# Kernel tuning notes

Hardware: AMD Instinct MI355X
Metric: run time of the kernel (lower is better)

Reference implementation:

```python
import jax, jax.numpy as jnp
import numpy as np

B, G, D, H, DH, L, M, FF = 8, 20000, 256, 8, 32, 4, 128, 1024
MASK_ID = -10.0


def _ortho(rng, m, d):
    # Gaussian orthogonal random features (performer_pytorch, scaling=0)
    rows = []
    n = 0
    while n < m:
        q, _ = np.linalg.qr(rng.standard_normal((d, d)))
        rows.append(q.T)
        n += d
    W = np.concatenate(rows)[:m]
    mult = np.linalg.norm(rng.standard_normal((m, d)), axis=1)
    return (mult[:, None] * W).astype(np.float32)


def setup_inputs() -> dict:
    rng = np.random.default_rng(0)
    p = lambda *s: (0.02 * rng.standard_normal(s)).astype(np.float32)
    z = lambda *s: np.zeros(s, np.float32)
    o = lambda *s: np.ones(s, np.float32)
    inp = dict(
        x=rng.standard_normal((B, G)).astype(np.float32),
        gene_emb=p(G, D),
        se_w1=p(G, 256), se_b1=z(256), se_w2=p(256, D), se_b2=z(D),
        proj_w1=p(D, FF), proj_b1=z(FF), proj_w2=p(FF, D), proj_b2=z(D),
        ln1_g=o(L, D), ln1_b=z(L, D),
        wq=p(L, D, D), wk=p(L, D, D), wv=p(L, D, D), wo=p(L, D, D), bo=z(L, D),
        ln2_g=o(L, D), ln2_b=z(L, D),
        ff_w1=p(L, D, FF), ff_b1=z(L, FF), ff_w2=p(L, FF, D), ff_b2=z(L, D),
        feat_proj=np.stack([_ortho(rng, M, DH) for _ in range(L)]),
        norm_g=o(D), norm_b=z(D),
        head_w1=p(D, FF), head_b1=z(FF), head_w2=p(FF, 1), head_b2=z(1),
    )
    return {k: jnp.asarray(v) for k, v in inp.items()}


def _ln(x, g, b, eps=1e-5):
    mu = jnp.mean(x, -1, keepdims=True)
    var = jnp.mean((x - mu) ** 2, -1, keepdims=True)
    return (x - mu) * jax.lax.rsqrt(var + eps) * g + b


def _softmax_kernel(x, proj, is_query, eps=1e-4):
    # FAVOR+ positive softmax kernel features (performer_pytorch softmax_kernel)
    d = x.shape[-1]
    ratio = proj.shape[0] ** -0.5
    dn = d ** -0.25
    dd = jnp.einsum('bhnd,md->bhnm', x * dn, proj)
    diag = 0.5 * jnp.sum(x * x, -1, keepdims=True) * (dn * dn)
    if is_query:
        m = jnp.max(dd, axis=-1, keepdims=True)
    else:
        m = jnp.max(dd, axis=(-1, -2), keepdims=True)
    return ratio * (jnp.exp(dd - diag - m) + eps)


def _forward(x, gene_emb, se_w1, se_b1, se_w2, se_b2, proj_w1, proj_b1,
             proj_w2, proj_b2, ln1_g, ln1_b, wq, wk, wv, wo, bo, ln2_g, ln2_b,
             ff_w1, ff_b1, ff_w2, ff_b2, feat_proj, norm_g, norm_b,
             head_w1, head_b1, head_w2, head_b2):
    # Rotary Expression Embedding
    inv_freq = 1.0 / (100.0 ** (jnp.arange(0, D, 2, dtype=jnp.float32) / D))
    freqs = x[:, :, None] * inv_freq                        # [B,G,D/2]
    ree = jnp.concatenate([jnp.sin(freqs), jnp.cos(freqs)], -1)
    ree = jnp.where((x == MASK_ID)[:, :, None], 0.0, ree)
    # sample embedding + gene token embedding
    samp = jax.nn.relu(x @ se_w1 + se_b1) @ se_w2 + se_b2   # [B,D]
    h = gene_emb[None] + ree + samp[:, None, :]             # [B,G,D]
    h = jax.nn.relu(h @ proj_w1 + proj_b1) @ proj_w2 + proj_b2
    for l in range(L):
        x0 = h
        a = _ln(x0, ln1_g[l], ln1_b[l])
        q = (a @ wq[l]).reshape(B, G, H, DH).transpose(0, 2, 1, 3)
        k = (a @ wk[l]).reshape(B, G, H, DH).transpose(0, 2, 1, 3)
        v = (a @ wv[l]).reshape(B, G, H, DH).transpose(0, 2, 1, 3)
        qp = _softmax_kernel(q, feat_proj[l], True)         # [B,H,G,M]
        kp = _softmax_kernel(k, feat_proj[l], False)
        ksum = kp.sum(2)                                    # [B,H,M]
        dinv = 1.0 / jnp.einsum('bhnm,bhm->bhn', qp, ksum)
        ctx = jnp.einsum('bhnm,bhnd->bhmd', kp, v)          # [B,H,M,DH]
        o_ = jnp.einsum('bhnm,bhmd,bhn->bhnd', qp, ctx, dinv)
        o_ = o_.transpose(0, 2, 1, 3).reshape(B, G, D)
        y = x0 + (o_ @ wo[l] + bo[l])                       # attn residual
        f = _ln(y, ln2_g[l], ln2_b[l])
        y = y + (jax.nn.gelu(f @ ff_w1[l] + ff_b1[l], approximate=False) @ ff_w2[l] + ff_b2[l])
        h = y + h                                           # outer residual
    h = _ln(h, norm_g, norm_b)
    pred = (jax.nn.relu(h @ head_w1 + head_b1) @ head_w2 + head_b2)[..., 0]
    return jax.nn.relu(pred)                                # [B,G]


def reference(x, gene_emb, se_w1, se_b1, se_w2, se_b2, proj_w1, proj_b1,
              proj_w2, proj_b2, ln1_g, ln1_b, wq, wk, wv, wo, bo, ln2_g,
              ln2_b, ff_w1, ff_b1, ff_w2, ff_b2, feat_proj, norm_g, norm_b,
              head_w1, head_b1, head_w2, head_b2):
    return _forward(x, gene_emb, se_w1, se_b1, se_w2, se_b2, proj_w1, proj_b1,
                    proj_w2, proj_b2, ln1_g, ln1_b, wq, wk, wv, wo, bo, ln2_g,
                    ln2_b, ff_w1, ff_b1, ff_w2, ff_b2, feat_proj, norm_g,
                    norm_b, head_w1, head_b1, head_w2, head_b2)
```

## Files before the change

### kernel.cpp

```cpp
#include <hip/hip_runtime.h>

#define Bb 8
#define Gg 20000
#define Dd 256
#define Hh 8
#define DHh 32
#define Ll 4
#define Mm 128
#define FFf 1024
#define QKVS 768
#define NBLK 192
#define NSLOT 105

typedef __attribute__((ext_vector_type(8))) short bf16x8;
typedef __attribute__((ext_vector_type(4))) float f32x4;

#define DN    0.4204482076268573f
#define DN2H  0.088388347648318447f
#define RATIO 0.08838834764831845f
#define EPSK  1e-4f

__device__ __forceinline__ float geluf(float x) {
    return 0.5f * x * (1.0f + erff(x * 0.70710678118654752f));
}
__device__ __forceinline__ float bf2f(ushort u) {
    union { uint i; float f; } v; v.i = ((uint)u) << 16; return v.f;
}
__device__ __forceinline__ ushort f2bf(float f) {
    union { float f; uint i; } v; v.f = f;
    uint i = v.i;
    return (ushort)((i + 0x7FFFu + ((i >> 16) & 1u)) >> 16);
}
__device__ __forceinline__ void gload16(const void* g, void* l) {
    __builtin_amdgcn_global_load_lds(
        (const __attribute__((address_space(1))) void*)g,
        (__attribute__((address_space(3))) void*)l, 16, 0, 0);
}

__global__ __launch_bounds__(256) void k_wt4(const float* __restrict__ wk,
    const float* __restrict__ wv, const float* __restrict__ wq,
    const float* __restrict__ wo, ushort* __restrict__ Wt)
{
    const int z = blockIdx.z, l = z >> 2, wh = z & 3;
    const float* src = (wh == 0) ? wk : (wh == 1) ? wv : (wh == 2) ? wq : wo;
    src += (size_t)l * 65536;
    ushort* d = Wt + (size_t)l * 786432 + (size_t)wh * 65536;
    __shared__ float tl[32][33];
    const int n0 = blockIdx.x * 32, k0 = blockIdx.y * 32;
    const int tx = threadIdx.x & 31, ty = threadIdx.x >> 5;
#pragma unroll
    for (int i = 0; i < 4; i++)
        tl[ty + i*8][tx] = src[(size_t)(k0 + ty + i*8) * 256 + n0 + tx];
    __syncthreads();
#pragma unroll
    for (int i = 0; i < 4; i++)
        d[(size_t)(n0 + ty + i*8) * 256 + k0 + tx] = f2bf(tl[tx][ty + i*8]);
}

__global__ __launch_bounds__(256) void k_wtA(const float* __restrict__ ff1,
    const float* __restrict__ pw1, const float* __restrict__ hw1,
    ushort* __restrict__ Wt)
{
    const int z = blockIdx.z;
    const float* src; ushort* d;
    if (z < 4)      { src = ff1 + (size_t)z*262144; d = Wt + (size_t)z*786432 + 262144; }
    else if (z == 4){ src = pw1; d = Wt + (size_t)4*786432; }
    else            { src = hw1; d = Wt + (size_t)4*786432 + 524288; }
    __shared__ float tl[32][33];
    const int n0 = blockIdx.x * 32, k0 = blockIdx.y * 32;
    const int tx = threadIdx.x & 31, ty = threadIdx.x >> 5;
#pragma unroll
    for (int i = 0; i < 4; i++)
        tl[ty + i*8][tx] = src[(size_t)(k0 + ty + i*8) * 1024 + n0 + tx];
    __syncthreads();
#pragma unroll
    for (int i = 0; i < 4; i++)
        d[(size_t)(n0 + ty + i*8) * 256 + k0 + tx] = f2bf(tl[tx][ty + i*8]);
}

__global__ __launch_bounds__(256) void k_wtB(const float* __restrict__ ff2,
    const float* __restrict__ pw2, ushort* __restrict__ Wt)
{
    const int z = blockIdx.z;
    const float* src; ushort* d;
    if (z < 4) { src = ff2 + (size_t)z*262144; d = Wt + (size_t)z*786432 + 524288; }
    else       { src = pw2; d = Wt + (size_t)4*786432 + 262144; }
    __shared__ float tl[32][33];
    const int n0 = blockIdx.x * 32, k0 = blockIdx.y * 32;
    const int tx = threadIdx.x & 31, ty = threadIdx.x >> 5;
#pragma unroll
    for (int i = 0; i < 4; i++)
        tl[ty + i*8][tx] = src[(size_t)(k0 + ty + i*8) * 256 + n0 + tx];
    __syncthreads();
#pragma unroll
    for (int i = 0; i < 4; i++)
        d[(size_t)(n0 + ty + i*8) * 1024 + k0 + tx] = f2bf(tl[tx][ty + i*8]);
}

__global__ __launch_bounds__(256) void k_pcast(const float* __restrict__ src,
    ushort* __restrict__ dst, int n)
{
    int i = blockIdx.x*256 + threadIdx.x;
    if (i < n) dst[i] = f2bf(src[i]);
}

__global__ __launch_bounds__(128) void k_pn(const float* __restrict__ featp,
    float* __restrict__ pnorm)
{
    const int l = blockIdx.x, t = threadIdx.x;
    const float* p = featp + (size_t)l*4096 + t*32;
    float s = 0.f;
#pragma unroll
    for (int d = 0; d < 32; d++) s += p[d]*p[d];
#pragma unroll
    for (int off = 1; off < 64; off <<= 1) s = fmaxf(s, __shfl_xor(s, off));
    __shared__ float sm2[2];
    if ((t & 63) == 0) sm2[t >> 6] = s;
    __syncthreads();
    if (t == 0) pnorm[l] = sqrtf(fmaxf(sm2[0], sm2[1]));
}

__global__ __launch_bounds__(512) void gemm_bf(
    const ushort* __restrict__ A, const ushort* __restrict__ Bt,
    const float* __restrict__ bias, ushort* __restrict__ C,
    int Mrows, int N, int K, int act)
{
    __shared__ ushort As[8192];
    __shared__ ushort Bs[8192];
    const int t = threadIdx.x;
    const int l = t & 63, wid = t >> 6;
    const int lr = l & 15, q = l >> 4;
    const int wm = wid >> 2, wn = wid & 3;
    const int row0 = blockIdx.y * 128, col0 = blockIdx.x * 128;

    const int sar = min(row0 + wid*16 + lr, Mrows - 1);
    const ushort* gA = A  + (size_t)sar * K + q*8;
    const ushort* gB = Bt + (size_t)(col0 + wid*16 + lr) * K + q*8;
    ushort* lA = As + wid*1024;
    ushort* lB = Bs + wid*1024;

    f32x4 acc[4][2] = {};

    for (int k0 = 0; k0 < K; k0 += 64) {
        __syncthreads();
        gload16(gA + k0,      lA);
        gload16(gA + k0 + 32, lA + 512);
        gload16(gB + k0,      lB);
        gload16(gB + k0 + 32, lB + 512);
        __syncthreads();
#pragma unroll
        for (int kg = 0; kg < 2; kg++) {
            bf16x8 af[4];
#pragma unroll
            for (int mi = 0; mi < 4; mi++)
                af[mi] = *(const bf16x8*)&As[((wm*4 + mi)*2 + kg)*512 + l*8];
#pragma unroll
            for (int ni = 0; ni < 2; ni++) {
                bf16x8 bv = *(const bf16x8*)&Bs[((wn*2 + ni)*2 + kg)*512 + l*8];
#pragma unroll
                for (int mi = 0; mi < 4; mi++)
                    acc[mi][ni] = __builtin_amdgcn_mfma_f32_16x16x32_bf16(
                        af[mi], bv, acc[mi][ni], 0, 0, 0);
            }
        }
    }

#pragma unroll
    for (int mi = 0; mi < 4; mi++)
#pragma unroll
        for (int j = 0; j < 4; j++) {
            int row = row0 + wm*64 + mi*16 + q*4 + j;
            if (row >= Mrows) continue;
#pragma unroll
            for (int ni = 0; ni < 2; ni++) {
                int col = col0 + wn*32 + ni*16 + lr;
                float v = acc[mi][ni][j];
                if (bias) v += bias[col];
                if (act == 1) v = fmaxf(v, 0.f);
                else if (act == 2) v = geluf(v);
                C[(size_t)row * N + col] = f2bf(v);
            }
        }
}

__global__ __launch_bounds__(512) void gemm_ln(
    const ushort* __restrict__ A, const ushort* __restrict__ Bt,
    const float* __restrict__ bias, const float* __restrict__ res,
    float* __restrict__ Cout, ushort* __restrict__ ABout,
    const float* __restrict__ gam, const float* __restrict__ bet,
    int Mrows, int K, int addC)
{
    __shared__ ushort As[4096];
    __shared__ ushort Bs[16384];
    __shared__ float red1[4][64], red2[4][64];
    const int t = threadIdx.x, l = t & 63, wid = t >> 6;
    const int lr = l & 15, lq = l >> 4;
    const int wm = wid >> 2, wn = wid & 3;
    const int row0 = blockIdx.x * 64;

    const int sar = min(row0 + (wid >> 1)*16 + lr, Mrows - 1);
    const ushort* gA = A + (size_t)sar * K + (wid & 1)*32 + lq*8;
    ushort* lA = As + wid*512;
    const ushort* gB[4];
    ushort* lB[4];
#pragma unroll
    for (int i = 0; i < 4; i++) {
        int g = wid*4 + i;
        gB[i] = Bt + (size_t)((g >> 1)*16 + lr) * K + (g & 1)*32 + lq*8;
        lB[i] = Bs + g*512;
    }

    f32x4 acc[2][4] = {};

    for (int k0 = 0; k0 < K; k0 += 64) {
        __syncthreads();
        gload16(gA + k0, lA);
#pragma unroll
        for (int i = 0; i < 4; i++) gload16(gB[i] + k0, lB[i]);
        __syncthreads();
#pragma unroll
        for (int kg = 0; kg < 2; kg++) {
            bf16x8 af[2];
#pragma unroll
            for (int mi = 0; mi < 2; mi++)
                af[mi] = *(const bf16x8*)&As[((wm*2 + mi)*2 + kg)*512 + l*8];
#pragma unroll
            for (int ni = 0; ni < 4; ni++) {
                bf16x8 bv = *(const bf16x8*)&Bs[((wn*4 + ni)*2 + kg)*512 + l*8];
#pragma unroll
                for (int mi = 0; mi < 2; mi++)
                    acc[mi][ni] = __builtin_amdgcn_mfma_f32_16x16x32_bf16(
                        af[mi], bv, acc[mi][ni], 0, 0, 0);
            }
        }
    }

    float biasv[4], gv[4], bvv[4];
#pragma unroll
    for (int ni = 0; ni < 4; ni++) {
        int col = wn*64 + ni*16 + lr;
        biasv[ni] = bias[col]; gv[ni] = gam[col]; bvv[ni] = bet[col];
    }
#pragma unroll
    for (int mi = 0; mi < 2; mi++)
#pragma unroll
        for (int j = 0; j < 4; j++) {
            int row = row0 + wm*32 + mi*16 + lq*4 + j;
            bool ok = row < Mrows;
#pragma unroll
            for (int ni = 0; ni < 4; ni++) {
                float v = acc[mi][ni][j] + biasv[ni];
                size_t ci = (size_t)row * 256 + wn*64 + ni*16 + lr;
                if (ok) {
                    if (res)  v += res[ci];
                    if (addC) v += Cout[ci];
                }
                acc[mi][ni][j] = v;
            }
        }
#pragma unroll
    for (int mi = 0; mi < 2; mi++)
#pragma unroll
        for (int j = 0; j < 4; j++) {
            float s1 = 0.f, s2 = 0.f;
#pragma unroll
            for (int ni = 0; ni < 4; ni++) {
                float v = acc[mi][ni][j];
                s1 += v; s2 += v*v;
            }
#pragma unroll
            for (int off = 1; off < 16; off <<= 1) {
                s1 += __shfl_xor(s1, off);
                s2 += __shfl_xor(s2, off);
            }
            if (lr == 0) {
                int r = wm*32 + mi*16 + lq*4 + j;
                red1[wn][r] = s1;
                red2[wn][r] = s2;
            }
        }
    __syncthreads();
#pragma unroll
    for (int mi = 0; mi < 2; mi++)
#pragma unroll
        for (int j = 0; j < 4; j++) {
            int r = wm*32 + mi*16 + lq*4 + j;
            int row = row0 + r;
            if (row >= Mrows) continue;
            float m1 = (red1[0][r]+red1[1][r]+red1[2][r]+red1[3][r]) * (1.f/256.f);
            float m2 = (red2[0][r]+red2[1][r]+red2[2][r]+red2[3][r]) * (1.f/256.f);
            float inv = rsqrtf(m2 - m1*m1 + 1e-5f);
#pragma unroll
            for (int ni = 0; ni < 4; ni++) {
                size_t ci = (size_t)row * 256 + wn*64 + ni*16 + lr;
                float v = acc[mi][ni][j];
                Cout[ci] = v;
                ABout[ci] = f2bf((v - m1)*inv*gv[ni] + bvv[ni]);
            }
        }
}

__global__ __launch_bounds__(256) void k_zero(float* __restrict__ p, int n) {
    int i = blockIdx.x*256 + threadIdx.x;
    if (i < n) p[i] = 0.f;
}

__global__ __launch_bounds__(256) void k_se1(const float* __restrict__ x,
    const float* __restrict__ w1, float* __restrict__ t1)
{
    const int blk = blockIdx.x, b = blockIdx.y, t = threadIdx.x;
    const int k0 = blk * 250;
    float acc = 0.f;
    for (int kk = 0; kk < 250; kk++) {
        float xv = x[b*Gg + k0 + kk];
        acc += xv * w1[(size_t)(k0 + kk)*256 + t];
    }
    atomicAdd(&t1[b*256 + t], acc);
}

__global__ __launch_bounds__(256) void k_se2(const float* __restrict__ t1,
    const float* __restrict__ b1, const float* __restrict__ w2,
    const float* __restrict__ b2, float* __restrict__ samp)
{
    const int b = blockIdx.x, t = threadIdx.x;
    __shared__ float s1[256];
    s1[t] = fmaxf(t1[b*256 + t] + b1[t], 0.f);
    __syncthreads();
    float acc = 0.f;
    for (int n = 0; n < 256; n++) acc += s1[n] * w2[(size_t)n*256 + t];
    samp[b*256 + t] = acc + b2[t];
}

__global__ __launch_bounds__(256) void k_embed(const float* __restrict__ x,
    const float* __restrict__ gene_emb, const float* __restrict__ samp,
    ushort* __restrict__ outb, int b0)
{
    const int w = threadIdx.x >> 6, l = threadIdx.x & 63;
    const int mb = blockIdx.x * 4 + w;
    const int bb = mb / Gg;
    const int g  = mb - bb * Gg;
    const int b  = b0 + bb;
    const float xv = x[b*Gg + g];
    const int d0 = l * 4;
    float4 gev = *(const float4*)&gene_emb[(size_t)g*256 + d0];
    float4 sv  = *(const float4*)&samp[b*256 + d0];
    float gv[4] = {gev.x, gev.y, gev.z, gev.w};
    float sp[4] = {sv.x, sv.y, sv.z, sv.w};
    ushort4 o;
    ushort* op = (ushort*)&o;
#pragma unroll
    for (int i = 0; i < 4; i++) {
        int d = d0 + i, j = d & 127;
        float ang = xv * __expf(-(float)j * 0.035977892078032f);
        float ree = (d < 128) ? __sinf(ang) : __cosf(ang);
        if (xv == -10.0f) ree = 0.f;
        op[i] = f2bf(gv[i] + ree + sp[i]);
    }
    *(ushort4*)&outb[(size_t)mb*256 + d0] = o;
}

__global__ __launch_bounds__(256) void k_ctx2(const ushort* __restrict__ qkv,
    const ushort* __restrict__ projb, const float* __restrict__ pnorm, int lidx,
    float* __restrict__ ctxp, float* __restrict__ ksp, float* __restrict__ svp,
    float* __restrict__ mlp)
{
    __shared__ ushort kpsT[128][72];
    __shared__ ushort vt[32][72];
    __shared__ float diag[192];
    __shared__ float sm[4];
    __shared__ float ksl[4][128];
    __shared__ float svl[8][32];
    const int bh = blockIdx.y, blk = blockIdx.x;
    const int h = bh & 7;
    const ushort* qkvb = qkv + (size_t)(bh >> 3) * Gg * QKVS;
    const int t = threadIdx.x, w = t >> 6, l = t & 63;
    const int lr = l & 15, lq = l >> 4;
    bf16x8 pb[8];
#pragma unroll
    for (int nt = 0; nt < 8; nt++)
        pb[nt] = *(const bf16x8*)(projb + (nt*16 + lr)*32 + lq*8);
    const int g0 = blk * NBLK;
    const int rows = min(NBLK, Gg - g0);
    f32x4 z = {};

    bf16x8 afs0 = {}, afs1 = {}, afs2 = {};
    float mx = 0.f;
    {
        int arow = min(g0 + w*16 + lr, Gg - 1);
        afs0 = *(const bf16x8*)(qkvb + (size_t)arow*QKVS + h*32 + lq*8);
        float s = 0.f;
#pragma unroll
        for (int j = 0; j < 8; j++) { float kv = bf2f((ushort)afs0[j]); s += kv*kv; }
        s += __shfl_xor(s, 16); s += __shfl_xor(s, 32);
        if (l < 16) diag[w*16 + l] = DN2H * s;
        mx = fmaxf(mx, s);
    }
    if (64 < rows) {
        int arow = min(g0 + 64 + w*16 + lr, Gg - 1);
        afs1 = *(const bf16x8*)(qkvb + (size_t)arow*QKVS + h*32 + lq*8);
        float s = 0.f;
#pragma unroll
        for (int j = 0; j < 8; j++) { float kv = bf2f((ushort)afs1[j]); s += kv*kv; }
        s += __shfl_xor(s, 16); s += __shfl_xor(s, 32);
        if (l < 16) diag[64 + w*16 + l] = DN2H * s;
        mx = fmaxf(mx, s);
    }
    if (128 < rows) {
        int arow = min(g0 + 128 + w*16 + lr, Gg - 1);
        afs2 = *(const bf16x8*)(qkvb + (size_t)arow*QKVS + h*32 + lq*8);
        float s = 0.f;
#pragma unroll
        for (int j = 0; j < 8; j++) { float kv = bf2f((ushort)afs2[j]); s += kv*kv; }
        s += __shfl_xor(s, 16); s += __shfl_xor(s, 32);
        if (l < 16) diag[128 + w*16 + l] = DN2H * s;
        mx = fmaxf(mx, s);
    }
#pragma unroll
    for (int off = 1; off < 64; off <<= 1) mx = fmaxf(mx, __shfl_xor(mx, off));
    if (l == 0) sm[w] = mx;
    __syncthreads();
    const float mloc = DN * sqrtf(fmaxf(fmaxf(sm[0], sm[1]), fmaxf(sm[2], sm[3])))
                     * pnorm[lidx];
    if (t == 0) mlp[bh*NSLOT + blk] = mloc;

    f32x4 cacc[2][2] = {};
    float ksacc[8] = {};
    float svacc = 0.f;
#pragma unroll
    for (int c = 0; c < 3; c++) {
        if (c*64 >= rows) break;
        bf16x8 af = (c == 0) ? afs0 : (c == 1) ? afs1 : afs2;
        const int nr = min(64, rows - c*64);
        const int rbase = g0 + c*64;
        f32x4 dd[8];
#pragma unroll
        for (int nt = 0; nt < 8; nt++)
            dd[nt] = __builtin_amdgcn_mfma_f32_16x16x32_bf16(af, pb[nt], z, 0, 0, 0);
        __syncthreads();
        float dg[4];
#pragma unroll
        for (int j = 0; j < 4; j++) dg[j] = diag[c*64 + w*16 + lq*4 + j];
#pragma unroll
        for (int nt = 0; nt < 8; nt++) {
            ushort4 kp4;
            ushort* kpp = (ushort*)&kp4;
#pragma unroll
            for (int j = 0; j < 4; j++) {
                int rj = w*16 + lq*4 + j;
                float e = 0.f;
                if (rj < nr) e = __expf(DN*dd[nt][j] - dg[j] - mloc);
                ksacc[nt] += e;
                kpp[j] = f2bf(e);
            }
            *(ushort4*)&kpsT[nt*16 + lr][w*16 + lq*4] = kp4;
        }
        for (int i = t; i < 512; i += 256) {
            int r = i >> 3, c4 = (i & 7) * 4;
            ushort4 vv = make_ushort4(0, 0, 0, 0);
            if (r < nr)
                vv = *(const ushort4*)(qkvb + (size_t)(rbase + r)*QKVS + 256 + h*32 + c4);
            vt[c4+0][r] = vv.x; vt[c4+1][r] = vv.y;
            vt[c4+2][r] = vv.z; vt[c4+3][r] = vv.w;
        }
        __syncthreads();
        {
            int dh = t & 31, gs = (t >> 5) * 8;
            float p = 0.f;
#pragma unroll
            for (int i = 0; i < 8; i++) p += bf2f(vt[dh][gs + i]);
            svacc += p;
        }
#pragma unroll
        for (int ks = 0; ks < 2; ks++) {
            bf16x8 a0 = *(const bf16x8*)&vt[lr][ks*32 + lq*8];
            bf16x8 a1 = *(const bf16x8*)&vt[16 + lr][ks*32 + lq*8];
#pragma unroll
            for (int ntp = 0; ntp < 2; ntp++) {
                bf16x8 bfr = *(const bf16x8*)&kpsT[(w*2 + ntp)*16 + lr][ks*32 + lq*8];
                cacc[0][ntp] = __builtin_amdgcn_mfma_f32_16x16x32_bf16(a0, bfr, cacc[0][ntp], 0, 0, 0);
                cacc[1][ntp] = __builtin_amdgcn_mfma_f32_16x16x32_bf16(a1, bfr, cacc[1][ntp], 0, 0, 0);
            }
        }
    }
    float* cslot = ctxp + (size_t)(bh*NSLOT + blk)*4096;
#pragma unroll
    for (int dt = 0; dt < 2; dt++)
#pragma unroll
        for (int ntp = 0; ntp < 2; ntp++)
#pragma unroll
            for (int j = 0; j < 4; j++)
                cslot[(dt*16 + lq*4 + j)*128 + (w*2 + ntp)*16 + lr] = cacc[dt][ntp][j];
#pragma unroll
    for (int nt = 0; nt < 8; nt++) {
        float v = ksacc[nt];
        v += __shfl_xor(v, 16); v += __shfl_xor(v, 32);
        if (l < 16) ksl[w][nt*16 + l] = v;
    }
    svl[t >> 5][t & 31] = svacc;
    __syncthreads();
    if (t < 128)
        ksp[(size_t)(bh*NSLOT + blk)*128 + t] = ksl[0][t] + ksl[1][t] + ksl[2][t] + ksl[3][t];
    if (t < 32) {
        float sv = 0.f;
#pragma unroll
        for (int i = 0; i < 8; i++) sv += svl[i][t];
        svp[(size_t)(bh*NSLOT + blk)*32 + t] = sv;
    }
}

__global__ __launch_bounds__(256) void k_cred2(const float* __restrict__ ctxp,
    const float* __restrict__ ksp, const float* __restrict__ svp,
    const float* __restrict__ mlp, ushort* __restrict__ ctxbg,
    float* __restrict__ ksum)
{
    __shared__ float mls[NSLOT];
    __shared__ float sc[NSLOT];
    __shared__ float svt[32];
    const int bh = blockIdx.y, blk = blockIdx.x, t = threadIdx.x;
    if (t < NSLOT) mls[t] = mlp[bh*NSLOT + t];
    __syncthreads();
    float km = -1e30f;
    for (int s = 0; s < NSLOT; s++) km = fmaxf(km, mls[s]);
    if (t < NSLOT) sc[t] = __expf(mls[t] - km);
    if (t < 32) {
        float sv = 0.f;
        for (int s = 0; s < NSLOT; s++) sv += svp[(size_t)(bh*NSLOT + s)*32 + t];
        svt[t] = sv;
    }
    __syncthreads();
    const int i = blk*256 + t;
    float acc = 0.f;
    for (int s = 0; s < NSLOT; s++)
        acc += sc[s] * ctxp[(size_t)(bh*NSLOT + s)*4096 + i];
    ctxbg[bh*4096 + i] = f2bf(RATIO * (acc + EPSK * svt[i >> 7]));
    if (blk == 0 && t < 128) {
        float ka = 0.f;
        for (int s = 0; s < NSLOT; s++)
            ka += sc[s] * ksp[(size_t)(bh*NSLOT + s)*128 + t];
        ksum[bh*128 + t] = RATIO * (ka + EPSK * (float)Gg);
    }
}

__global__ __launch_bounds__(256) void k_attn(const ushort* __restrict__ qkv,
    const ushort* __restrict__ projb, const ushort* __restrict__ ctxbg,
    const float* __restrict__ ksum, ushort* __restrict__ obuf)
{
    __shared__ ushort qps[64][136];
    __shared__ float ksl[128];
    __shared__ float dgq[64];
    const int bh = blockIdx.y, blk = blockIdx.x;
    const int h = bh & 7;
    const ushort* qkvb = qkv + (size_t)(bh >> 3) * Gg * QKVS;
    ushort* obufb = obuf + (size_t)(bh >> 3) * Gg * 256;
    const int t = threadIdx.x, w = t >> 6, l = t & 63;
    const int lr = l & 15, lq = l >> 4;
    bf16x8 pb[8];
#pragma unroll
    for (int nt = 0; nt < 8; nt++)
        pb[nt] = *(const bf16x8*)(projb + (nt*16 + lr)*32 + lq*8);
    if (t < 128) ksl[t] = ksum[bh*128 + t];
    bf16x8 cb[2][4];
#pragma unroll
    for (int dt = 0; dt < 2; dt++)
#pragma unroll
        for (int ks = 0; ks < 4; ks++)
            cb[dt][ks] = *(const bf16x8*)(ctxbg + bh*4096 + (dt*16 + lr)*128 + ks*32 + lq*8);
    __syncthreads();
    const int g0 = blk * NBLK;
    const int rows = min(NBLK, Gg - g0);
    f32x4 z = {};
    for (int gc = 0; gc < rows; gc += 64) {
        const int nr = min(64, rows - gc);
        const int rbase = g0 + gc;
        int arow = min(rbase + w*16 + lr, Gg - 1);
        bf16x8 af = *(const bf16x8*)(qkvb + (size_t)arow*QKVS + 512 + h*32 + lq*8);
        float s = 0.f;
#pragma unroll
        for (int j = 0; j < 8; j++) { float qv = bf2f((ushort)af[j]); s += qv*qv; }
        s += __shfl_xor(s, 16); s += __shfl_xor(s, 32);
        if (l < 16) dgq[w*16 + l] = DN2H * s;
        f32x4 dd[8];
#pragma unroll
        for (int nt = 0; nt < 8; nt++)
            dd[nt] = __builtin_amdgcn_mfma_f32_16x16x32_bf16(af, pb[nt], z, 0, 0, 0);
        __syncthreads();
        float dg[4], mq[4], den[4], dinv[4];
#pragma unroll
        for (int j = 0; j < 4; j++) {
            dg[j] = dgq[w*16 + lq*4 + j];
            float m = -1e30f;
#pragma unroll
            for (int nt = 0; nt < 8; nt++) m = fmaxf(m, dd[nt][j]);
            mq[j] = m;
        }
#pragma unroll
        for (int off = 1; off < 16; off <<= 1)
#pragma unroll
            for (int j = 0; j < 4; j++) mq[j] = fmaxf(mq[j], __shfl_xor(mq[j], off));
#pragma unroll
        for (int j = 0; j < 4; j++) { mq[j] = DN*mq[j]; den[j] = 0.f; }
#pragma unroll
        for (int nt = 0; nt < 8; nt++) {
            float kv = ksl[nt*16 + lr];
#pragma unroll
            for (int j = 0; j < 4; j++) {
                float p = RATIO * (__expf(DN*dd[nt][j] - dg[j] - mq[j]) + EPSK);
                dd[nt][j] = p;
                den[j] += p * kv;
            }
        }
#pragma unroll
        for (int off = 1; off < 16; off <<= 1)
#pragma unroll
            for (int j = 0; j < 4; j++) den[j] += __shfl_xor(den[j], off);
#pragma unroll
        for (int j = 0; j < 4; j++) dinv[j] = 1.f / den[j];
#pragma unroll
        for (int nt = 0; nt < 8; nt++)
#pragma unroll
            for (int j = 0; j < 4; j++)
                qps[w*16 + lq*4 + j][nt*16 + lr] = f2bf(dd[nt][j]);
        __syncthreads();
        f32x4 oacc[2] = {};
#pragma unroll
        for (int ks = 0; ks < 4; ks++) {
            bf16x8 aq = *(const bf16x8*)&qps[w*16 + lr][ks*32 + lq*8];
            oacc[0] = __builtin_amdgcn_mfma_f32_16x16x32_bf16(aq, cb[0][ks], oacc[0], 0, 0, 0);
            oacc[1] = __builtin_amdgcn_mfma_f32_16x16x32_bf16(aq, cb[1][ks], oacc[1], 0, 0, 0);
        }
#pragma unroll
        for (int dt = 0; dt < 2; dt++)
#pragma unroll
            for (int j = 0; j < 4; j++) {
                int rj = w*16 + lq*4 + j;
                if (rj < nr)
                    obufb[(size_t)(rbase + rj)*256 + h*32 + dt*16 + lr]
                        = f2bf(oacc[dt][j] * dinv[j]);
            }
    }
}

__global__ __launch_bounds__(512) void k_headd(const ushort* __restrict__ u,
    const float* __restrict__ w2, const float* __restrict__ b2,
    float* __restrict__ outp, int Mrows)
{
    const int w = threadIdx.x >> 6, l = threadIdx.x & 63;
    const int row = blockIdx.x * 8 + w;
    if (row >= Mrows) return;
    const ushort* up = u + (size_t)row * 1024 + l * 16;
    const float*  wp = w2 + l * 16;
    float acc = 0.f;
#pragma unroll
    for (int i = 0; i < 2; i++) {
        uint4 uv = *(const uint4*)(up + i*8);
        const ushort* us = (const ushort*)&uv;
        float4 w0 = *(const float4*)(wp + i*8);
        float4 w1 = *(const float4*)(wp + i*8 + 4);
        acc += bf2f(us[0])*w0.x + bf2f(us[1])*w0.y
             + bf2f(us[2])*w0.z + bf2f(us[3])*w0.w
             + bf2f(us[4])*w1.x + bf2f(us[5])*w1.y
             + bf2f(us[6])*w1.z + bf2f(us[7])*w1.w;
    }
#pragma unroll
    for (int off = 1; off < 64; off <<= 1) acc += __shfl_xor(acc, off);
    if (l == 0) outp[row] = fmaxf(acc + b2[0], 0.f);
}

extern "C" void kernel_launch(void* const* d_in, const int* in_sizes, int n_in,
                              void* d_out, int out_size, void* d_ws, size_t ws_size,
                              hipStream_t stream)
{
    const float* x        = (const float*)d_in[0];
    const float* gene_emb = (const float*)d_in[1];
    const float* se_w1    = (const float*)d_in[2];
    const float* se_b1    = (const float*)d_in[3];
    const float* se_w2    = (const float*)d_in[4];
    const float* se_b2    = (const float*)d_in[5];
    const float* proj_b1  = (const float*)d_in[7];
    const float* proj_b2  = (const float*)d_in[9];
    const float* ln1_g    = (const float*)d_in[10];
    const float* ln1_b    = (const float*)d_in[11];
    const float* bo       = (const float*)d_in[16];
    const float* ln2_g    = (const float*)d_in[17];
    const float* ln2_b    = (const float*)d_in[18];
    const float* ff_b1    = (const float*)d_in[20];
    const float* ff_b2    = (const float*)d_in[22];
    const float* featp    = (const float*)d_in[23];
    const float* norm_g   = (const float*)d_in[24];
    const float* norm_b   = (const float*)d_in[25];
    const float* head_b1  = (const float*)d_in[27];
    const float* head_w2  = (const float*)d_in[28];
    const float* head_b2  = (const float*)d_in[29];
    const float* wq  = (const float*)d_in[12];
    const float* wk  = (const float*)d_in[13];
    const float* wv  = (const float*)d_in[14];
    const float* wo  = (const float*)d_in[15];
    const float* ff_w1 = (const float*)d_in[19];
    const float* ff_w2 = (const float*)d_in[21];
    const float* proj_w1 = (const float*)d_in[6];
    const float* proj_w2 = (const float*)d_in[8];
    const float* head_w1 = (const float*)d_in[26];
    float* out = (float*)d_out;

    const int NBP  = (ws_size >= (size_t)185000000) ? 2 : 1;
    const int MB   = NBP * Gg;
    const int CHKF = (NBP == 2 && ws_size >= (size_t)210000000) ? 40000
                   : (NBP == 2 || ws_size >= (size_t)102000000) ? 20000 : 10000;
    const int NCHF = MB / CHKF;
    const int NPASS = Bb / NBP;

    float* w = (float*)d_ws;
    const size_t SBm = (size_t)MB * Dd;
    float* f_h  = w;
    float* B1   = w + SBm;
    float* samp = w + 2*SBm;
    float* t1   = samp + 2048;
    float* ksum = t1 + 2048;
    ushort* ctxbg = (ushort*)(ksum + NBP*1024);
    float* pnormb = (float*)(ctxbg + NBP*32768);
    ushort* Ab  = (ushort*)(w + 2*SBm + 40000);
    ushort* U   = Ab + SBm;
    const size_t usz = (size_t)MB * QKVS > (size_t)CHKF * FFf
                     ? (size_t)MB * QKVS : (size_t)CHKF * FFf;
    ushort* Wt  = U + usz;
    ushort* projb = Wt + 3932160;
    ushort* QKVb = U;
    ushort* B4   = U;
    float* ctxp = B1;
    float* ksp  = B1 + (size_t)NBP*NSLOT*8*4096;
    float* svp  = ksp + (size_t)NBP*NSLOT*8*128;
    float* mlp  = svp + (size_t)NBP*NSLOT*8*32;

    const size_t LW = 786432;
    ushort* pj1T = Wt + 4*LW;
    ushort* pj2T = pj1T + 262144;
    ushort* hd1T = pj2T + 262144;

    auto gemmb = [&](const ushort* A, const ushort* Bt, const float* bias,
                     ushort* C, int Mr, int N, int K, int act) {
        gemm_bf<<<dim3(N/128, (Mr + 127)/128), 512, 0, stream>>>(A, Bt, bias, C, Mr, N, K, act);
    };
    auto gemml = [&](const ushort* A, const ushort* Bt, const float* bias,
                     const float* res, float* Cout, ushort* ABout,
                     const float* g, const float* be, int Mr, int K, int addC) {
        gemm_ln<<<dim3((Mr + 63)/64), 512, 0, stream>>>(A, Bt, bias, res, Cout, ABout,
                                                        g, be, Mr, K, addC);
    };

    k_wt4<<<dim3(8, 8, 16), 256, 0, stream>>>(wk, wv, wq, wo, Wt);
    k_wtA<<<dim3(32, 8, 6), 256, 0, stream>>>(ff_w1, proj_w1, head_w1, Wt);
    k_wtB<<<dim3(8, 32, 5), 256, 0, stream>>>(ff_w2, proj_w2, Wt);
    k_pcast<<<64, 256, 0, stream>>>(featp, projb, Ll*Mm*DHh);
    k_pn<<<4, 128, 0, stream>>>(featp, pnormb);
    k_zero<<<8, 256, 0, stream>>>(t1, 2048);
    k_se1<<<dim3(80, 8), 256, 0, stream>>>(x, se_w1, t1);
    k_se2<<<8, 256, 0, stream>>>(t1, se_b1, se_w2, se_b2, samp);

    for (int p = 0; p < NPASS; p++) {
        k_embed<<<MB/4, 256, 0, stream>>>(x, gene_emb, samp, Ab, p*NBP);
        for (int c = 0; c < NCHF; c++) {
            size_t off = (size_t)c * CHKF * Dd;
            gemmb(Ab + off, pj1T, proj_b1, B4, CHKF, FFf, Dd, 1);
            gemml(B4, pj2T, proj_b2, nullptr, f_h + off, Ab + off,
                  ln1_g, ln1_b, CHKF, FFf, 0);
        }
        for (int l = 0; l < Ll; l++) {
            ushort* lw = Wt + (size_t)l * LW;
            const ushort* qkvT = lw;
            const ushort* oT   = lw + 196608;
            const ushort* f1T  = lw + 262144;
            const ushort* f2T  = lw + 524288;
            const ushort* pjb  = projb + (size_t)l*Mm*DHh;
            const float* gn = (l < Ll-1) ? ln1_g + (l+1)*Dd : norm_g;
            const float* bn = (l < Ll-1) ? ln1_b + (l+1)*Dd : norm_b;

            gemmb(Ab, qkvT, nullptr, QKVb, MB, QKVS, Dd, 0);
            k_ctx2<<<dim3(NSLOT, 8*NBP), 256, 0, stream>>>(QKVb, pjb, pnormb, l,
                                                           ctxp, ksp, svp, mlp);
            k_cred2<<<dim3(16, 8*NBP), 256, 0, stream>>>(ctxp, ksp, svp, mlp,
                                                         ctxbg, ksum);
            k_attn<<<dim3(NSLOT, 8*NBP), 256, 0, stream>>>(QKVb, pjb, ctxbg, ksum, Ab);
            gemml(Ab, oT, bo + l*Dd, f_h, B1, Ab,
                  ln2_g + l*Dd, ln2_b + l*Dd, MB, Dd, 0);
            for (int c = 0; c < NCHF; c++) {
                size_t off = (size_t)c * CHKF * Dd;
                gemmb(Ab + off, f1T, ff_b1 + l*FFf, B4, CHKF, FFf, Dd, 2);
                gemml(B4, f2T, ff_b2 + l*Dd, B1 + off, f_h + off, Ab + off,
                      gn, bn, CHKF, FFf, 1);
            }
        }
        gemmb(Ab, hd1T, head_b1, B4, MB, FFf, Dd, 1);
        k_headd<<<(MB + 7)/8, 512, 0, stream>>>(B4, head_w2, head_b2,
                                                out + (size_t)p*MB, MB);
    }
}
```

Before: 6.100 ms.

## Double-buffer LDS tiles in gemm_ln with async prefetch two chunks ahead

Turns the gemm_ln K-loop into a double-buffered pipeline. The next two K-chunks are prefetched into alternate LDS buffers, and explicit vmcnt waits plus raw barriers replace the two __syncthreads per iteration, so global loads overlap the MFMA work. The LayerNorm reduction scratch now reuses the A buffer, which offsets the extra shared memory from doubling the buffers. The cost is higher LDS use per block, which can lower occupancy, and a dependence on the exact count of outstanding loads for correctness.

```diff
diff --git a/kernel.cpp b/kernel.cpp
--- a/kernel.cpp
+++ b/kernel.cpp
@@ -190,9 +190,8 @@
     const float* __restrict__ gam, const float* __restrict__ bet,
     int Mrows, int K, int addC)
 {
-    __shared__ ushort As[4096];
-    __shared__ ushort Bs[16384];
-    __shared__ float red1[4][64], red2[4][64];
+    __shared__ ushort As[2][4096];
+    __shared__ ushort Bs[2][16384];
     const int t = threadIdx.x, l = t & 63, wid = t >> 6;
     const int lr = l & 15, lq = l >> 4;
     const int wm = wid >> 2, wn = wid & 3;
@@ -200,40 +199,63 @@
 
     const int sar = min(row0 + (wid >> 1)*16 + lr, Mrows - 1);
     const ushort* gA = A + (size_t)sar * K + (wid & 1)*32 + lq*8;
-    ushort* lA = As + wid*512;
     const ushort* gB[4];
-    ushort* lB[4];
 #pragma unroll
     for (int i = 0; i < 4; i++) {
         int g = wid*4 + i;
         gB[i] = Bt + (size_t)((g >> 1)*16 + lr) * K + (g & 1)*32 + lq*8;
-        lB[i] = Bs + g*512;
     }
 
     f32x4 acc[2][4] = {};
-
-    for (int k0 = 0; k0 < K; k0 += 64) {
-        __syncthreads();
-        gload16(gA + k0, lA);
-#pragma unroll
-        for (int i = 0; i < 4; i++) gload16(gB[i] + k0, lB[i]);
-        __syncthreads();
+    const int nk = K >> 6;
+
+    gload16(gA, As[0] + wid*512);
+#pragma unroll
+    for (int i = 0; i < 4; i++) gload16(gB[i], Bs[0] + (wid*4 + i)*512);
+    if (nk > 1) {
+        gload16(gA + 64, As[1] + wid*512);
+#pragma unroll
+        for (int i = 0; i < 4; i++) gload16(gB[i] + 64, Bs[1] + (wid*4 + i)*512);
+    }
+
+    for (int c = 0; c < nk; c++) {
+        if (c < nk - 1) asm volatile("s_waitcnt vmcnt(5)" ::: "memory");
+        else            asm volatile("s_waitcnt vmcnt(0)" ::: "memory");
+        __builtin_amdgcn_sched_barrier(0);
+        __builtin_amdgcn_s_barrier();
+        __builtin_amdgcn_sched_barrier(0);
+        const ushort* Ap = As[c & 1];
+        const ushort* Bp = Bs[c & 1];
 #pragma unroll
         for (int kg = 0; kg < 2; kg++) {
             bf16x8 af[2];
 #pragma unroll
             for (int mi = 0; mi < 2; mi++)
-                af[mi] = *(const bf16x8*)&As[((wm*2 + mi)*2 + kg)*512 + l*8];
+                af[mi] = *(const bf16x8*)&Ap[((wm*2 + mi)*2 + kg)*512 + l*8];
 #pragma unroll
             for (int ni = 0; ni < 4; ni++) {
-                bf16x8 bv = *(const bf16x8*)&Bs[((wn*4 + ni)*2 + kg)*512 + l*8];
+                bf16x8 bv = *(const bf16x8*)&Bp[((wn*4 + ni)*2 + kg)*512 + l*8];
 #pragma unroll
                 for (int mi = 0; mi < 2; mi++)
                     acc[mi][ni] = __builtin_amdgcn_mfma_f32_16x16x32_bf16(
                         af[mi], bv, acc[mi][ni], 0, 0, 0);
             }
         }
-    }
+        __builtin_amdgcn_sched_barrier(0);
+        __builtin_amdgcn_s_barrier();
+        __builtin_amdgcn_sched_barrier(0);
+        if (c + 2 < nk) {
+            int ko = (c + 2) * 64;
+            gload16(gA + ko, As[c & 1] + wid*512);
+#pragma unroll
+            for (int i = 0; i < 4; i++)
+                gload16(gB[i] + ko, Bs[c & 1] + (wid*4 + i)*512);
+        }
+    }
+
+    __syncthreads();
+    float* red1 = (float*)(&As[0][0]);
+    float* red2 = red1 + 256;
 
     float biasv[4], gv[4], bvv[4];
 #pragma unroll
@@ -275,8 +297,8 @@
             }
             if (lr == 0) {
                 int r = wm*32 + mi*16 + lq*4 + j;
-                red1[wn][r] = s1;
-                red2[wn][r] = s2;
+                red1[wn*64 + r] = s1;
+                red2[wn*64 + r] = s2;
             }
         }
     __syncthreads();
@@ -287,8 +309,8 @@
             int r = wm*32 + mi*16 + lq*4 + j;
             int row = row0 + r;
             if (row >= Mrows) continue;
-            float m1 = (red1[0][r]+red1[1][r]+red1[2][r]+red1[3][r]) * (1.f/256.f);
-            float m2 = (red2[0][r]+red2[1][r]+red2[2][r]+red2[3][r]) * (1.f/256.f);
+            float m1 = (red1[r]+red1[64+r]+red1[128+r]+red1[192+r]) * (1.f/256.f);
+            float m2 = (red2[r]+red2[64+r]+red2[128+r]+red2[192+r]) * (1.f/256.f);
             float inv = rsqrtf(m2 - m1*m1 + 1e-5f);
 #pragma unroll
             for (int ni = 0; ni < 4; ni++) {
```

Measured after the change: 6.594 ms. 1.08x slower.
